# Performance work log

Measured on AMD Instinct MI355X. Metric: run time of the kernel, lower is better.

Reference implementation:

```python
import jax, jax.numpy as jnp
import numpy as np

T = 1024      # series length (hourly)
S = 168       # weekly seasonality period
H = 128       # hidden size
WIN = 168     # input window
OUT = 24      # forecast horizon
N = T - WIN - OUT + 1  # 833 windows
STD = 1e-3    # label/input log-noise std


def setup_inputs() -> dict:
    key = jax.random.key(0)
    ks = jax.random.split(key, 16)
    s = 1.0 / np.sqrt(H)
    u = lambda k, shape, lo, hi: jax.random.uniform(k, shape, jnp.float32, lo, hi)
    return {
        # strictly positive series (log is taken of normalized values)
        "x": u(ks[0], (T,), 0.5, 1.5),
        "lvl_smooth_raw": u(ks[1], (), -1.0, 1.0),      # Uniform(-1,1) init, sigmoid applied
        "seas_smooth_raw": u(ks[2], (), -1.0, 1.0),
        "seas_params_raw": u(ks[3], (S,), 0.65, 1.35),  # exp applied in forward
        "noise_in": jax.random.normal(ks[4], (N, WIN), jnp.float32) * STD,
        "noise_lab": jax.random.normal(ks[5], (N, OUT), jnp.float32) * STD,
        "lstm_Wx0": u(ks[6], (4 * H, 1), -s, s),
        "lstm_Wh0": u(ks[7], (4 * H, H), -s, s),
        "lstm_b0": u(ks[8], (4 * H,), -s, s),
        "lstm_Wx1": u(ks[9], (4 * H, H), -s, s),
        "lstm_Wh1": u(ks[10], (4 * H, H), -s, s),
        "lstm_b1": u(ks[11], (4 * H,), -s, s),
        "tanh_W": u(ks[12], (H, H), -s, s),
        "tanh_b": u(ks[13], (H,), -s, s),
        "lin_W": u(ks[14], (OUT, H), -s, s),
        "lin_b": u(ks[15], (OUT,), -s, s),
        "window_size": WIN,
        "output_size": OUT,
    }


def _es_scan(x, a, g, w_init):
    """Holt-Winters-style level/seasonality recurrence as a lax.scan.

    Mirrors the original loop: at step i it reads w_seasons[i] (lag-S circular
    buffer, with w_seasons[S] aliased to w_seasons[0]) and appends the updated
    seasonal factor at index S+i. Returns levels[0:T] and w_seasons[0:T].
    """
    Sn = w_init.shape[0]
    level0 = x[0] / w_init[0]

    def step(carry, i):
        level, buf = carry
        j = jnp.mod(i, Sn)
        w = buf[j]
        nl = a * x[i] / w + (1.0 - a) * level
        nw = g * x[i] / nl + (1.0 - g) * w
        buf = buf.at[j].set(nw)
        return (nl, buf), (nl, nw)

    (_, _), (lvls, nws) = jax.lax.scan(step, (level0, w_init), jnp.arange(1, x.shape[0]))
    levels = jnp.concatenate([level0[None], lvls])                      # [T]
    ws_full = jnp.concatenate([w_init, w_init[:1], nws])[: x.shape[0]]  # [T]
    return levels, ws_full


def _lstm_layer(xs, Wx, Wh, b):
    """xs: [W, N, in] -> (hidden sequence [W, N, H], final hidden [N, H]). Torch gate order i,f,g,o."""
    Hn = Wh.shape[1]
    h0 = jnp.zeros((xs.shape[1], Hn), xs.dtype)

    def step(carry, xt):
        h, c = carry
        gates = xt @ Wx.T + h @ Wh.T + b  # [N, 4H]
        i_, f_, g_, o_ = jnp.split(gates, 4, axis=-1)
        c = jax.nn.sigmoid(f_) * c + jax.nn.sigmoid(i_) * jnp.tanh(g_)
        h = jax.nn.sigmoid(o_) * jnp.tanh(c)
        return (h, c), h

    (h, _), hs = jax.lax.scan(step, (h0, h0), xs)
    return hs, h


def reference(x, lvl_smooth_raw, seas_smooth_raw, seas_params_raw, noise_in, noise_lab,
              lstm_Wx0, lstm_Wh0, lstm_b0, lstm_Wx1, lstm_Wh1, lstm_b1,
              tanh_W, tanh_b, lin_W, lin_b, window_size, output_size):
    a = jax.nn.sigmoid(lvl_smooth_raw)
    g = jax.nn.sigmoid(seas_smooth_raw)
    w_init = jnp.exp(seas_params_raw)

    levels, ws = _es_scan(x, a, g, w_init)

    n = x.shape[0] - window_size - output_size + 1
    iw = jnp.arange(n)[:, None] + jnp.arange(window_size)[None, :]
    il = jnp.arange(n)[:, None] + window_size + jnp.arange(output_size)[None, :]  # [N, OUT]
    lev = levels[jnp.arange(n) + window_size][:, None]                          # [N, 1]

    sq_in = jnp.log(x[iw] / (lev * ws[iw])) + noise_in       # deseasonalized, log-squashed, noisy
    labels = jnp.log(x[il] / (lev * ws[il])) + noise_lab

    # DRNN over the window dimension, batch = windows; take last-layer final hidden.
    xs = jnp.transpose(sq_in)[:, :, None]
    hs0, _ = _lstm_layer(xs, lstm_Wx0, lstm_Wh0, lstm_b0)
    _, h = _lstm_layer(hs0, lstm_Wx1, lstm_Wh1, lstm_b1)     # [N, H]

    feat = jnp.tanh(h @ tanh_W.T + tanh_b)                   # non_lin.Tanh(H, H)
    out = feat @ lin_W.T + lin_b                             # [N, OUT]
    level_var_loss = jnp.float32(0.0)                        # lvp = 0 default
    return out, labels, level_var_loss
```

## Files before the change

kernel.cpp:

```cpp
#include <hip/hip_runtime.h>
#include <math.h>

#define T_LEN   1024
#define S_SEAS  168
#define H_SZ    128
#define G_SZ    512
#define WIN_SZ  168
#define OUT_SZ  24
#define N_WIN   833
#define BB      16
#define NBLK    ((N_WIN + BB - 1) / BB)
#define NPAD    (NBLK * BB)

typedef __attribute__((ext_vector_type(8))) __bf16 bf16x8;
typedef __attribute__((ext_vector_type(4))) float  f32x4;

__device__ __forceinline__ float fsig(float x) {
    return __fdividef(1.0f, 1.0f + __expf(-x));
}
__device__ __forceinline__ float ftanh(float x) {
    return 1.0f - __fdividef(2.0f, __expf(2.0f * x) + 1.0f);
}

#define LDS_BARRIER()                                        \
    do {                                                     \
        asm volatile("s_waitcnt lgkmcnt(0)" ::: "memory");   \
        __builtin_amdgcn_s_barrier();                        \
    } while (0)

__global__ __launch_bounds__(256) void pre_kernel(
    const float* __restrict__ x,
    const float* __restrict__ lvl_raw,
    const float* __restrict__ seas_raw,
    const float* __restrict__ seas_params,
    const float* __restrict__ Wh0,
    const float* __restrict__ Wx1,
    const float* __restrict__ Wh1,
    const float* __restrict__ tanhW,
    float* __restrict__ levels,
    float* __restrict__ wsv,
    uint4* __restrict__ pw0,
    uint4* __restrict__ pw1,
    float* __restrict__ tanhWT) {
    const int t = threadIdx.x;

    if (blockIdx.x == 0) {
        __shared__ float xl[T_LEN];
        __shared__ float buf[S_SEAS];
        __shared__ float Ss[S_SEAS], Fs[S_SEAS];
        __shared__ float levCarry;
        for (int i = t; i < T_LEN; i += 256) xl[i] = x[i];
        for (int i = t; i < S_SEAS; i += 256) {
            const float w = expf(seas_params[i]);
            buf[i] = w;
            wsv[i] = w;
        }
        __syncthreads();
        const float a  = 1.0f / (1.0f + expf(-lvl_raw[0]));
        const float g  = 1.0f / (1.0f + expf(-seas_raw[0]));
        const float ca = 1.0f - a, cg = 1.0f - g;
        if (t == 0) {
            levCarry = __fdividef(xl[0], buf[0]);
            levels[0] = levCarry;
            wsv[S_SEAS] = buf[0];
        }
        __syncthreads();

        int cs = 1;
        while (cs < T_LEN) {
            const int L = min(S_SEAS, T_LEN - cs);
            float w = 0.0f;
            if (t < L) {
                const int i = cs + t;
                w = buf[i % S_SEAS];
                Ss[t] = __fdividef(a * xl[i], w);
                Fs[t] = ca;
            }
            __syncthreads();
            for (int d = 1; d < L; d <<= 1) {
                float sp = 0.0f, fp = 0.0f;
                const bool act = (t < L) && (t >= d);
                if (act) { sp = Ss[t - d]; fp = Fs[t - d]; }
                __syncthreads();
                if (act) {
                    Ss[t] = Ss[t] + Fs[t] * sp;
                    Fs[t] = Fs[t] * fp;
                }
                __syncthreads();
            }
            if (t < L) {
                const int i = cs + t;
                const float nl = Ss[t] + Fs[t] * levCarry;
                levels[i] = nl;
                const float nw = cg * w + __fdividef(g * xl[i], nl);
                buf[i % S_SEAS] = nw;
                if (i + S_SEAS < T_LEN) wsv[i + S_SEAS] = nw;
            }
            __syncthreads();
            if (t == 0) levCarry = Ss[L - 1] + Fs[L - 1] * levCarry;
            __syncthreads();
            cs += L;
        }
        return;
    }

    const int idx = (blockIdx.x - 1) * 256 + t;
    auto bfr = [](float f) -> unsigned int {
        union { float f; unsigned int u; } v; v.f = f;
        return ((v.u + 0x7FFFu + ((v.u >> 16) & 1u)) >> 16) & 0xFFFFu;
    };
    if (idx < 8192) {
        const int l = idx & 63, f = idx >> 6;
        const int kt = f & 3, ns = (f >> 2) & 3, w = f >> 4;
        const int g = ns * 128 + w * 16 + (l & 15);
        const int kb = kt * 32 + (l >> 4) * 8;
        const float* s = Wh0 + g * H_SZ + kb;
        uint4 o;
        unsigned int* po = &o.x;
        for (int p = 0; p < 4; ++p) po[p] = bfr(s[2 * p]) | (bfr(s[2 * p + 1]) << 16);
        pw0[idx] = o;
    } else if (idx < 8192 + 16384) {
        const int j = idx - 8192;
        const int l = j & 63, f = j >> 6;
        const int kt = f & 7, ns = (f >> 3) & 3, w = f >> 5;
        const int g = ns * 128 + w * 16 + (l & 15);
        const float* srcm = (kt < 4) ? Wx1 : Wh1;
        const int kb = (kt & 3) * 32 + (l >> 4) * 8;
        const float* s = srcm + g * H_SZ + kb;
        uint4 o;
        unsigned int* po = &o.x;
        for (int p = 0; p < 4; ++p) po[p] = bfr(s[2 * p]) | (bfr(s[2 * p + 1]) << 16);
        pw1[j] = o;
    } else if (idx < 8192 + 16384 + 16384) {
        const int j = idx - 8192 - 16384;
        const int m = j >> 7, k = j & 127;
        tanhWT[k * H_SZ + m] = tanhW[j];
    }
}

__global__ __launch_bounds__(512, 2) void lstm_pipe_kernel(
    const float* __restrict__ x,
    const float* __restrict__ levels,
    const float* __restrict__ wsv,
    const float* __restrict__ noise_in,
    const float* __restrict__ Wx0,
    const float* __restrict__ b0v,
    const uint4* __restrict__ pw0,
    const float* __restrict__ b1v,
    const uint4* __restrict__ pw1,
    const float* __restrict__ tanhWT,
    const float* __restrict__ tanhB,
    const float* __restrict__ linW,
    const float* __restrict__ linB,
    const float* __restrict__ noise_lab,
    __bf16* __restrict__ hs0,
    unsigned* __restrict__ flag,
    float* __restrict__ out) {
    __shared__ union {
        struct { __bf16 h0s[2][16 * 128]; float xls[WIN_SZ][16]; } a;
        struct { __bf16 h1s[2][16 * 128]; float hfl[16][129]; float featl[16][128]; } b;
    } sm;
    __shared__ unsigned flagLDS;

    const int tid  = threadIdx.x;
    const int w    = tid >> 6;
    const int lane = tid & 63;
    const int cc   = lane & 15;
    const int kl   = lane >> 4;

    int rdA[4], wrA[4];
#pragma unroll
    for (int kt = 0; kt < 4; ++kt)
        rdA[kt] = cc * 256 + ((kt * 64 + kl * 16) ^ ((cc & 7) << 4));
#pragma unroll
    for (int r = 0; r < 4; ++r) {
        const int row = kl * 4 + r;
        wrA[r] = row * 256 + (((w * 16 + cc) * 2) ^ ((row & 7) << 4));
    }

    if (blockIdx.x < NBLK) {
        const int base = blockIdx.x * BB;

        for (int i = tid; i < WIN_SZ * BB; i += 512) {
            const int t = i >> 4, m = i & 15;
            const int nn = base + m;
            float v = 0.0f;
            if (nn < N_WIN) {
                const float lev = levels[nn + WIN_SZ];
                const int tt = nn + t;
                v = logf(x[tt] / (lev * wsv[tt])) + noise_in[nn * WIN_SZ + t];
            }
            sm.a.xls[t][m] = v;
        }
        for (int i = tid; i < 2 * 16 * 128; i += 512) (&sm.a.h0s[0][0])[i] = (__bf16)0.0f;

        const bf16x8* p0 = (const bf16x8*)pw0;
        bf16x8 wB0[4][4];
#pragma unroll
        for (int ns = 0; ns < 4; ++ns)
#pragma unroll
            for (int kt = 0; kt < 4; ++kt)
                wB0[ns][kt] = p0[((w * 4 + ns) * 4 + kt) * 64 + lane];
#pragma unroll
        for (int ns = 0; ns < 4; ++ns)
#pragma unroll
            for (int kt = 0; kt < 4; ++kt)
                asm("" : "+a"(wB0[ns][kt]));

        float b0r[4], wx0r[4];
#pragma unroll
        for (int ns = 0; ns < 4; ++ns) {
            const int g = ns * 128 + w * 16 + cc;
            b0r[ns]  = b0v[g];
            wx0r[ns] = Wx0[g];
        }
        float c0r[4] = {0.f, 0.f, 0.f, 0.f};
        int goff[4];
#pragma unroll
        for (int r = 0; r < 4; ++r)
            goff[r] = (base + kl * 4 + r) * H_SZ + w * 16 + cc;
        __syncthreads();

        char* const hb0 = (char*)&sm.a.h0s[0][0];

#define L0_STEP(T, P, PUBF)                                                    \
    {                                                                          \
        const int t_ = (T);                                                    \
        const float4 xt_ = *(const float4*)&sm.a.xls[t_][kl * 4];              \
        const float xa_[4] = {xt_.x, xt_.y, xt_.z, xt_.w};                     \
        f32x4 a0_, a1_, a2_, a3_;                                              \
        _Pragma("unroll")                                                      \
        for (int r = 0; r < 4; ++r) {                                          \
            a0_[r] = b0r[0] + wx0r[0] * xa_[r];                                \
            a1_[r] = b0r[1] + wx0r[1] * xa_[r];                                \
            a2_[r] = b0r[2] + wx0r[2] * xa_[r];                                \
            a3_[r] = b0r[3] + wx0r[3] * xa_[r];                                \
        }                                                                      \
        _Pragma("unroll")                                                      \
        for (int kt = 0; kt < 4; ++kt) {                                       \
            const bf16x8 af_ = *(const bf16x8*)(hb0 + (P) * 4096 + rdA[kt]);   \
            a0_ = __builtin_amdgcn_mfma_f32_16x16x32_bf16(af_, wB0[0][kt], a0_, 0, 0, 0); \
            a1_ = __builtin_amdgcn_mfma_f32_16x16x32_bf16(af_, wB0[1][kt], a1_, 0, 0, 0); \
            a2_ = __builtin_amdgcn_mfma_f32_16x16x32_bf16(af_, wB0[2][kt], a2_, 0, 0, 0); \
            a3_ = __builtin_amdgcn_mfma_f32_16x16x32_bf16(af_, wB0[3][kt], a3_, 0, 0, 0); \
        }                                                                      \
        const int off_ = t_ * (NPAD * H_SZ);                                   \
        _Pragma("unroll")                                                      \
        for (int r = 0; r < 4; ++r) {                                          \
            const float ig_ = fsig(a0_[r]);                                    \
            const float fg_ = fsig(a1_[r]);                                    \
            const float gg_ = ftanh(a2_[r]);                                   \
            const float og_ = fsig(a3_[r]);                                    \
            const float c_  = fg_ * c0r[r] + ig_ * gg_;                        \
            c0r[r] = c_;                                                       \
            const __bf16 hb_ = (__bf16)(og_ * ftanh(c_));                      \
            *(__bf16*)(hb0 + (((P) ^ 1) * 4096) + wrA[r]) = hb_;               \
            hs0[off_ + goff[r]] = hb_;                                         \
        }                                                                      \
        if (PUBF) {                                                            \
            asm volatile("s_waitcnt vmcnt(0) lgkmcnt(0)" ::: "memory");        \
            __builtin_amdgcn_s_barrier();                                      \
            if (tid == 0) {                                                    \
                __builtin_amdgcn_fence(__ATOMIC_RELEASE, "agent");             \
                __hip_atomic_store(flag + blockIdx.x, (unsigned)(t_ + 1),      \
                                   __ATOMIC_RELAXED, __HIP_MEMORY_SCOPE_AGENT);\
            }                                                                  \
        } else {                                                               \
            LDS_BARRIER();                                                     \
        }                                                                      \
    }

        for (int tp = 0; tp < WIN_SZ / 2; ++tp) {
            L0_STEP(2 * tp, 0, false)
            L0_STEP(2 * tp + 1, 1, ((tp & 3) == 3))
        }
#undef L0_STEP
    } else {
        const int bb   = blockIdx.x - NBLK;
        const int base = bb * BB;

        for (int i = tid; i < 2 * 16 * 128; i += 512) (&sm.b.h1s[0][0])[i] = (__bf16)0.0f;

        const bf16x8* p1 = (const bf16x8*)pw1;
        bf16x8 wX[4][4], wH[4][4];
#pragma unroll
        for (int ns = 0; ns < 4; ++ns)
#pragma unroll
            for (int kt = 0; kt < 4; ++kt) {
                wX[ns][kt] = p1[((w * 4 + ns) * 8 + kt) * 64 + lane];
                wH[ns][kt] = p1[((w * 4 + ns) * 8 + kt + 4) * 64 + lane];
            }
#pragma unroll
        for (int ns = 0; ns < 4; ++ns)
#pragma unroll
            for (int kt = 0; kt < 4; ++kt) {
                asm("" : "+a"(wX[ns][kt]));
                asm("" : "+a"(wH[ns][kt]));
            }

        float b1r[4];
#pragma unroll
        for (int ns = 0; ns < 4; ++ns) b1r[ns] = b1v[ns * 128 + w * 16 + cc];
        float c1r[4] = {0.f, 0.f, 0.f, 0.f};
        unsigned lastAcq = 0;

        {
            const unsigned need_ = 2;
            if (tid == 0) {
                unsigned v;
                for (;;) {
                    v = __hip_atomic_load(flag + bb, __ATOMIC_RELAXED,
                                          __HIP_MEMORY_SCOPE_AGENT);
                    if (v >= need_) break;
                    __builtin_amdgcn_s_sleep(8);
                }
                flagLDS = v;
                __builtin_amdgcn_fence(__ATOMIC_ACQUIRE, "agent");
            }
            __syncthreads();
            lastAcq = flagLDS;
        }

        const size_t arow = (size_t)(base + cc) * H_SZ + kl * 8;
        bf16x8 fA0 = *(const bf16x8*)&hs0[arow + 0];
        bf16x8 fA1 = *(const bf16x8*)&hs0[arow + 32];
        bf16x8 fA2 = *(const bf16x8*)&hs0[arow + 64];
        bf16x8 fA3 = *(const bf16x8*)&hs0[arow + 96];
        bf16x8 fB0, fB1, fB2, fB3;
        __syncthreads();

        char* const hb1 = (char*)&sm.b.h1s[0][0];

#define L1_STEP(T, P, C0, C1, C2, C3, N0, N1, N2, N3)                          \
    {                                                                          \
        const int t_ = (T);                                                    \
        const unsigned need_ =                                                 \
            (unsigned)((t_ + 2 < WIN_SZ) ? (t_ + 2) : WIN_SZ);                 \
        if (lastAcq < need_) {                                                 \
            if (tid == 0) {                                                    \
                unsigned v_;                                                   \
                for (;;) {                                                     \
                    v_ = __hip_atomic_load(flag + bb, __ATOMIC_RELAXED,        \
                                           __HIP_MEMORY_SCOPE_AGENT);          \
                    if (v_ >= need_) break;                                    \
                    __builtin_amdgcn_s_sleep(8);                               \
                }                                                              \
                flagLDS = v_;                                                  \
                __builtin_amdgcn_fence(__ATOMIC_ACQUIRE, "agent");             \
            }                                                                  \
            __syncthreads();                                                   \
            lastAcq = flagLDS;                                                 \
        }                                                                      \
        const int tn_ = (t_ + 1 < WIN_SZ) ? (t_ + 1) : (WIN_SZ - 1);           \
        const __bf16* p_ = hs0 + (size_t)tn_ * (NPAD * H_SZ) + arow;           \
        N0 = *(const bf16x8*)(p_);                                             \
        N1 = *(const bf16x8*)(p_ + 32);                                        \
        N2 = *(const bf16x8*)(p_ + 64);                                        \
        N3 = *(const bf16x8*)(p_ + 96);                                        \
        f32x4 a0_ = {b1r[0], b1r[0], b1r[0], b1r[0]};                          \
        f32x4 a1_ = {b1r[1], b1r[1], b1r[1], b1r[1]};                          \
        f32x4 a2_ = {b1r[2], b1r[2], b1r[2], b1r[2]};                          \
        f32x4 a3_ = {b1r[3], b1r[3], b1r[3], b1r[3]};                          \
        a0_ = __builtin_amdgcn_mfma_f32_16x16x32_bf16(C0, wX[0][0], a0_, 0, 0, 0); \
        a1_ = __builtin_amdgcn_mfma_f32_16x16x32_bf16(C0, wX[1][0], a1_, 0, 0, 0); \
        a2_ = __builtin_amdgcn_mfma_f32_16x16x32_bf16(C0, wX[2][0], a2_, 0, 0, 0); \
        a3_ = __builtin_amdgcn_mfma_f32_16x16x32_bf16(C0, wX[3][0], a3_, 0, 0, 0); \
        a0_ = __builtin_amdgcn_mfma_f32_16x16x32_bf16(C1, wX[0][1], a0_, 0, 0, 0); \
        a1_ = __builtin_amdgcn_mfma_f32_16x16x32_bf16(C1, wX[1][1], a1_, 0, 0, 0); \
        a2_ = __builtin_amdgcn_mfma_f32_16x16x32_bf16(C1, wX[2][1], a2_, 0, 0, 0); \
        a3_ = __builtin_amdgcn_mfma_f32_16x16x32_bf16(C1, wX[3][1], a3_, 0, 0, 0); \
        a0_ = __builtin_amdgcn_mfma_f32_16x16x32_bf16(C2, wX[0][2], a0_, 0, 0, 0); \
        a1_ = __builtin_amdgcn_mfma_f32_16x16x32_bf16(C2, wX[1][2], a1_, 0, 0, 0); \
        a2_ = __builtin_amdgcn_mfma_f32_16x16x32_bf16(C2, wX[2][2], a2_, 0, 0, 0); \
        a3_ = __builtin_amdgcn_mfma_f32_16x16x32_bf16(C2, wX[3][2], a3_, 0, 0, 0); \
        a0_ = __builtin_amdgcn_mfma_f32_16x16x32_bf16(C3, wX[0][3], a0_, 0, 0, 0); \
        a1_ = __builtin_amdgcn_mfma_f32_16x16x32_bf16(C3, wX[1][3], a1_, 0, 0, 0); \
        a2_ = __builtin_amdgcn_mfma_f32_16x16x32_bf16(C3, wX[2][3], a2_, 0, 0, 0); \
        a3_ = __builtin_amdgcn_mfma_f32_16x16x32_bf16(C3, wX[3][3], a3_, 0, 0, 0); \
        _Pragma("unroll")                                                      \
        for (int kt = 0; kt < 4; ++kt) {                                       \
            const bf16x8 af_ = *(const bf16x8*)(hb1 + (P) * 4096 + rdA[kt]);   \
            a0_ = __builtin_amdgcn_mfma_f32_16x16x32_bf16(af_, wH[0][kt], a0_, 0, 0, 0); \
            a1_ = __builtin_amdgcn_mfma_f32_16x16x32_bf16(af_, wH[1][kt], a1_, 0, 0, 0); \
            a2_ = __builtin_amdgcn_mfma_f32_16x16x32_bf16(af_, wH[2][kt], a2_, 0, 0, 0); \
            a3_ = __builtin_amdgcn_mfma_f32_16x16x32_bf16(af_, wH[3][kt], a3_, 0, 0, 0); \
        }                                                                      \
        _Pragma("unroll")                                                      \
        for (int r = 0; r < 4; ++r) {                                          \
            const float ig_ = fsig(a0_[r]);                                    \
            const float fg_ = fsig(a1_[r]);                                    \
            const float gg_ = ftanh(a2_[r]);                                   \
            const float og_ = fsig(a3_[r]);                                    \
            const float c_  = fg_ * c1r[r] + ig_ * gg_;                        \
            c1r[r] = c_;                                                       \
            const float hv_ = og_ * ftanh(c_);                                 \
            if (t_ == WIN_SZ - 1) {                                            \
                sm.b.hfl[kl * 4 + r][w * 16 + cc] = hv_;                       \
            } else {                                                           \
                *(__bf16*)(hb1 + (((P) ^ 1) * 4096) + wrA[r]) = (__bf16)hv_;   \
            }                                                                  \
        }                                                                      \
        LDS_BARRIER();                                                         \
    }

        for (int tp = 0; tp < WIN_SZ / 2; ++tp) {
            L1_STEP(2 * tp, 0, fA0, fA1, fA2, fA3, fB0, fB1, fB2, fB3)
            L1_STEP(2 * tp + 1, 1, fB0, fB1, fB2, fB3, fA0, fA1, fA2, fA3)
        }
#undef L1_STEP

        for (int p = tid; p < BB * H_SZ; p += 512) {
            const int m = p >> 7, u = p & 127;
            float acc = tanhB[u];
            for (int k = 0; k < H_SZ; ++k)
                acc += sm.b.hfl[m][k] * tanhWT[k * H_SZ + u];
            sm.b.featl[m][u] = tanhf(acc);
        }
        LDS_BARRIER();

        for (int p = tid; p < BB * OUT_SZ; p += 512) {
            const int m = p / OUT_SZ, o = p % OUT_SZ;
            const int nn = base + m;
            if (nn < N_WIN) {
                float acc = linB[o];
                for (int k = 0; k < H_SZ; ++k)
                    acc += sm.b.featl[m][k] * linW[o * H_SZ + k];
                out[nn * OUT_SZ + o] = acc;
                const float lev = levels[nn + WIN_SZ];
                const int tt = nn + WIN_SZ + o;
                out[N_WIN * OUT_SZ + nn * OUT_SZ + o] =
                    logf(x[tt] / (lev * wsv[tt])) + noise_lab[nn * OUT_SZ + o];
            }
        }
        if (bb == 0 && tid == 0)
            out[2 * N_WIN * OUT_SZ] = 0.0f;
    }
}

extern "C" void kernel_launch(void* const* d_in, const int* in_sizes, int n_in,
                              void* d_out, int out_size, void* d_ws, size_t ws_size,
                              hipStream_t stream) {
    const float* x           = (const float*)d_in[0];
    const float* lvl_raw     = (const float*)d_in[1];
    const float* seas_raw    = (const float*)d_in[2];
    const float* seas_params = (const float*)d_in[3];
    const float* noise_in    = (const float*)d_in[4];
    const float* noise_lab   = (const float*)d_in[5];
    const float* Wx0         = (const float*)d_in[6];
    const float* Wh0         = (const float*)d_in[7];
    const float* b0v         = (const float*)d_in[8];
    const float* Wx1         = (const float*)d_in[9];
    const float* Wh1         = (const float*)d_in[10];
    const float* b1v         = (const float*)d_in[11];
    const float* tanhW       = (const float*)d_in[12];
    const float* tanhB       = (const float*)d_in[13];
    const float* linW        = (const float*)d_in[14];
    const float* linB        = (const float*)d_in[15];
    float* out = (float*)d_out;

    float* wsf    = (float*)d_ws;
    float* levels = wsf;
    float* wsv    = levels + T_LEN;
    float* tanhWT = wsv + T_LEN;
    uint4* pw0    = (uint4*)(tanhWT + H_SZ * H_SZ);
    uint4* pw1    = pw0 + 8192;
    __bf16* hs0   = (__bf16*)(pw1 + 16384);
    unsigned* flags = (unsigned*)(hs0 + (size_t)WIN_SZ * NPAD * H_SZ);

    hipMemsetAsync(flags, 0, NBLK * sizeof(unsigned), stream);

    hipLaunchKernelGGL(pre_kernel, dim3(161), dim3(256), 0, stream,
                       x, lvl_raw, seas_raw, seas_params, Wh0, Wx1, Wh1, tanhW,
                       levels, wsv, pw0, pw1, tanhWT);
    hipLaunchKernelGGL(lstm_pipe_kernel, dim3(2 * NBLK), dim3(512), 0, stream,
                       x, levels, wsv, noise_in, Wx0, b0v, pw0,
                       b1v, pw1, tanhWT, tanhB, linW, linB, noise_lab,
                       hs0, flags, out);
}
```

Baseline: 357.7 us.

## Pin LSTM weight fragments in AGPRs via inline-asm MFMA and publish flags more often

Replaces the MFMA builtins in both LSTM layer loops with inline asm that takes the B (weight) operand from AGPRs. This frees VGPRs, since the resident weight fragments no longer need to sit in architectural registers. Manual s_nop guards are added before and after the MFMA sequences because the compiler cannot insert hazard waits around opaque asm. The layer-0 producer also publishes its progress flag every 4 timesteps instead of every 8, so the layer-1 consumer can start sooner, at the cost of more global fences and barriers.

```diff
diff --git a/kernel.cpp b/kernel.cpp
--- a/kernel.cpp
+++ b/kernel.cpp
@@ -22,11 +22,19 @@
     return 1.0f - __fdividef(2.0f, __expf(2.0f * x) + 1.0f);
 }
 
+__device__ __forceinline__ void mfma_av(f32x4& d, const bf16x8 a, const bf16x8 b) {
+    asm("v_mfma_f32_16x16x32_bf16 %0, %1, %2, %0"
+        : "+v"(d) : "v"(a), "a"(b));
+}
+
 #define LDS_BARRIER()                                        \
     do {                                                     \
         asm volatile("s_waitcnt lgkmcnt(0)" ::: "memory");   \
         __builtin_amdgcn_s_barrier();                        \
     } while (0)
+
+#define MFMA_PRE_GUARD()  asm volatile("s_nop 1")
+#define MFMA_POST_GUARD() asm volatile("s_nop 7\n\ts_nop 7")
 
 __global__ __launch_bounds__(256) void pre_kernel(
     const float* __restrict__ x,
@@ -236,14 +244,16 @@
             a2_[r] = b0r[2] + wx0r[2] * xa_[r];                                \
             a3_[r] = b0r[3] + wx0r[3] * xa_[r];                                \
         }                                                                      \
+        MFMA_PRE_GUARD();                                                      \
         _Pragma("unroll")                                                      \
         for (int kt = 0; kt < 4; ++kt) {                                       \
             const bf16x8 af_ = *(const bf16x8*)(hb0 + (P) * 4096 + rdA[kt]);   \
-            a0_ = __builtin_amdgcn_mfma_f32_16x16x32_bf16(af_, wB0[0][kt], a0_, 0, 0, 0); \
-            a1_ = __builtin_amdgcn_mfma_f32_16x16x32_bf16(af_, wB0[1][kt], a1_, 0, 0, 0); \
-            a2_ = __builtin_amdgcn_mfma_f32_16x16x32_bf16(af_, wB0[2][kt], a2_, 0, 0, 0); \
-            a3_ = __builtin_amdgcn_mfma_f32_16x16x32_bf16(af_, wB0[3][kt], a3_, 0, 0, 0); \
-        }                                                                      \
+            mfma_av(a0_, af_, wB0[0][kt]);                                     \
+            mfma_av(a1_, af_, wB0[1][kt]);                                     \
+            mfma_av(a2_, af_, wB0[2][kt]);                                     \
+            mfma_av(a3_, af_, wB0[3][kt]);                                     \
+        }                                                                      \
+        MFMA_POST_GUARD();                                                     \
         const int off_ = t_ * (NPAD * H_SZ);                                   \
         _Pragma("unroll")                                                      \
         for (int r = 0; r < 4; ++r) {                                          \
@@ -272,7 +282,7 @@
 
         for (int tp = 0; tp < WIN_SZ / 2; ++tp) {
             L0_STEP(2 * tp, 0, false)
-            L0_STEP(2 * tp + 1, 1, ((tp & 3) == 3))
+            L0_STEP(2 * tp + 1, 1, ((tp & 1) == 1))
         }
 #undef L0_STEP
     } else {
@@ -361,30 +371,32 @@
         f32x4 a1_ = {b1r[1], b1r[1], b1r[1], b1r[1]};                          \
         f32x4 a2_ = {b1r[2], b1r[2], b1r[2], b1r[2]};                          \
         f32x4 a3_ = {b1r[3], b1r[3], b1r[3], b1r[3]};                          \
-        a0_ = __builtin_amdgcn_mfma_f32_16x16x32_bf16(C0, wX[0][0], a0_, 0, 0, 0); \
-        a1_ = __builtin_amdgcn_mfma_f32_16x16x32_bf16(C0, wX[1][0], a1_, 0, 0, 0); \
-        a2_ = __builtin_amdgcn_mfma_f32_16x16x32_bf16(C0, wX[2][0], a2_, 0, 0, 0); \
-        a3_ = __builtin_amdgcn_mfma_f32_16x16x32_bf16(C0, wX[3][0], a3_, 0, 0, 0); \
-        a0_ = __builtin_amdgcn_mfma_f32_16x16x32_bf16(C1, wX[0][1], a0_, 0, 0, 0); \
-        a1_ = __builtin_amdgcn_mfma_f32_16x16x32_bf16(C1, wX[1][1], a1_, 0, 0, 0); \
-        a2_ = __builtin_amdgcn_mfma_f32_16x16x32_bf16(C1, wX[2][1], a2_, 0, 0, 0); \
-        a3_ = __builtin_amdgcn_mfma_f32_16x16x32_bf16(C1, wX[3][1], a3_, 0, 0, 0); \
-        a0_ = __builtin_amdgcn_mfma_f32_16x16x32_bf16(C2, wX[0][2], a0_, 0, 0, 0); \
-        a1_ = __builtin_amdgcn_mfma_f32_16x16x32_bf16(C2, wX[1][2], a1_, 0, 0, 0); \
-        a2_ = __builtin_amdgcn_mfma_f32_16x16x32_bf16(C2, wX[2][2], a2_, 0, 0, 0); \
-        a3_ = __builtin_amdgcn_mfma_f32_16x16x32_bf16(C2, wX[3][2], a3_, 0, 0, 0); \
-        a0_ = __builtin_amdgcn_mfma_f32_16x16x32_bf16(C3, wX[0][3], a0_, 0, 0, 0); \
-        a1_ = __builtin_amdgcn_mfma_f32_16x16x32_bf16(C3, wX[1][3], a1_, 0, 0, 0); \
-        a2_ = __builtin_amdgcn_mfma_f32_16x16x32_bf16(C3, wX[2][3], a2_, 0, 0, 0); \
-        a3_ = __builtin_amdgcn_mfma_f32_16x16x32_bf16(C3, wX[3][3], a3_, 0, 0, 0); \
+        MFMA_PRE_GUARD();                                                      \
+        mfma_av(a0_, C0, wX[0][0]);                                            \
+        mfma_av(a1_, C0, wX[1][0]);                                            \
+        mfma_av(a2_, C0, wX[2][0]);                                            \
+        mfma_av(a3_, C0, wX[3][0]);                                            \
+        mfma_av(a0_, C1, wX[0][1]);                                            \
+        mfma_av(a1_, C1, wX[1][1]);                                            \
+        mfma_av(a2_, C1, wX[2][1]);                                            \
+        mfma_av(a3_, C1, wX[3][1]);                                            \
+        mfma_av(a0_, C2, wX[0][2]);                                            \
+        mfma_av(a1_, C2, wX[1][2]);                                            \
+        mfma_av(a2_, C2, wX[2][2]);                                            \
+        mfma_av(a3_, C2, wX[3][2]);                                            \
+        mfma_av(a0_, C3, wX[0][3]);                                            \
+        mfma_av(a1_, C3, wX[1][3]);                                            \
+        mfma_av(a2_, C3, wX[2][3]);                                            \
+        mfma_av(a3_, C3, wX[3][3]);                                            \
         _Pragma("unroll")                                                      \
         for (int kt = 0; kt < 4; ++kt) {                                       \
             const bf16x8 af_ = *(const bf16x8*)(hb1 + (P) * 4096 + rdA[kt]);   \
-            a0_ = __builtin_amdgcn_mfma_f32_16x16x32_bf16(af_, wH[0][kt], a0_, 0, 0, 0); \
-            a1_ = __builtin_amdgcn_mfma_f32_16x16x32_bf16(af_, wH[1][kt], a1_, 0, 0, 0); \
-            a2_ = __builtin_amdgcn_mfma_f32_16x16x32_bf16(af_, wH[2][kt], a2_, 0, 0, 0); \
-            a3_ = __builtin_amdgcn_mfma_f32_16x16x32_bf16(af_, wH[3][kt], a3_, 0, 0, 0); \
-        }                                                                      \
+            mfma_av(a0_, af_, wH[0][kt]);                                      \
+            mfma_av(a1_, af_, wH[1][kt]);                                      \
+            mfma_av(a2_, af_, wH[2][kt]);                                      \
+            mfma_av(a3_, af_, wH[3][kt]);                                      \
+        }                                                                      \
+        MFMA_POST_GUARD();                                                     \
         _Pragma("unroll")                                                      \
         for (int r = 0; r < 4; ++r) {                                          \
             const float ig_ = fsig(a0_[r]);                                    \
```

Result: faster. 349.4 us (-2.3%).
